# Performance work log

Measured on AMD Instinct MI355X. Metric: run time of the kernel, lower is better.

The kernel has to match this reference:

```python
import jax, jax.numpy as jnp
import numpy as np

N = 10000; E = 320000
DIM = 176; ATT = 16; SH_HEADS = 16; TH = 4; NH = SH_HEADS + TH; VD = DIM // SH_HEADS
LMAX = 3; NSPH = (LMAX + 1) ** 2; ZDIM = 16; RDIM = 16
RSTART = 0.8; CUT = 5.0; NLAYERS = 2


def _ln(x):
    mu = jnp.mean(x, axis=-1, keepdims=True)
    dx = x - mu
    var = jnp.mean(dx ** 2, axis=-1, keepdims=True)
    return dx * (1e-6 + var) ** (-0.5)


def _sph(v):
    # real spherical harmonics up to l=3, unnormalized overall scale, [E,16]
    x, y, z = v[..., 0], v[..., 1], v[..., 2]
    s3 = np.float32(np.sqrt(3.0)); s15 = np.float32(np.sqrt(15.0))
    c1 = np.float32(np.sqrt(5.0 / 8.0)); c2 = np.float32(np.sqrt(3.0 / 8.0))
    x2, y2, z2 = x * x, y * y, z * z
    return jnp.stack([
        jnp.ones_like(x),
        x, y, z,
        s3 * x * y, s3 * y * z, 0.5 * (3.0 * z2 - 1.0), s3 * x * z, 0.5 * s3 * (x2 - y2),
        c1 * y * (3.0 * x2 - y2), s15 * x * y * z, c2 * y * (5.0 * z2 - 1.0),
        0.5 * z * (5.0 * z2 - 3.0), c2 * x * (5.0 * z2 - 1.0),
        0.5 * s15 * z * (x2 - y2), c1 * x * (x2 - 3.0 * y2),
    ], axis=-1)


def setup_inputs() -> dict:
    key = jax.random.key(0)
    ks = jax.random.split(key, 32)

    def rn(k, shape):
        fan_in = shape[0] if len(shape) > 1 else shape[0]
        return jax.random.normal(k, shape, dtype=jnp.float32) / np.float32(np.sqrt(shape[0]))

    species = jax.random.randint(ks[0], (N,), 0, 64)
    edge_src = jax.random.randint(ks[1], (E,), 0, N)
    edge_dst = jax.random.randint(ks[2], (E,), 0, N)
    distances = RSTART + (CUT - RSTART) * jax.random.uniform(ks[3], (E,), dtype=jnp.float32)
    raw = jax.random.normal(ks[4], (E, 3), dtype=jnp.float32)
    dirn = raw / jnp.linalg.norm(raw, axis=-1, keepdims=True)
    vec = dirn * distances[:, None]
    switch = 0.5 * (jnp.cos(jnp.pi * distances / CUT) + 1.0)

    inp = {
        'species': species, 'distances': distances, 'switch': switch,
        'edge_src': edge_src, 'edge_dst': edge_dst, 'vec': vec,
        'z_table': jax.random.normal(ks[5], (64, ZDIM), dtype=jnp.float32),
        'w_species': rn(ks[6], (ZDIM, DIM)),
        'pos_w1_0': rn(ks[7], (RDIM, 2 * ATT)), 'pos_b1_0': jnp.zeros((2 * ATT,), jnp.float32),
        'pos_w2_0': rn(ks[8], (2 * ATT, ATT)), 'pos_b2_0': jnp.zeros((ATT,), jnp.float32),
        'wq_0': rn(ks[9], (DIM, NH * ATT)), 'wk_0': rn(ks[10], (DIM, NH * ATT)),
        'wv_0': rn(ks[11], (DIM, SH_HEADS * VD)),
        'upd_w_0': rn(ks[12], (2 * DIM, DIM)), 'upd_b_0': jnp.zeros((DIM,), jnp.float32),
        'pos_w1_1': rn(ks[13], (RDIM + TH * (LMAX + 1), 2 * ATT)), 'pos_b1_1': jnp.zeros((2 * ATT,), jnp.float32),
        'pos_w2_1': rn(ks[14], (2 * ATT, ATT)), 'pos_b2_1': jnp.zeros((ATT,), jnp.float32),
        'wq_1': rn(ks[15], (DIM, NH * ATT)), 'wk_1': rn(ks[16], (DIM, NH * ATT)),
        'wv_1': rn(ks[17], (DIM, SH_HEADS * VD)),
        'upd_w_1': rn(ks[18], (2 * DIM, DIM)), 'upd_b_1': jnp.zeros((DIM,), jnp.float32),
    }
    return inp


def reference(species, distances, switch, edge_src, edge_dst, vec,
              z_table, w_species,
              pos_w1_0, pos_b1_0, pos_w2_0, pos_b2_0, wq_0, wk_0, wv_0, upd_w_0, upd_b_0,
              pos_w1_1, pos_b1_1, pos_w2_1, pos_b2_1, wq_1, wk_1, wv_1, upd_w_1, upd_b_1):
    Nn = species.shape[0]
    Zi = z_table[species]                      # [N, ZDIM] species encoding
    xi = _ln(Zi @ w_species)                   # [N, DIM]

    vhat = vec / distances[:, None]
    Yij = _sph(vhat)                           # [E, NSPH]
    ls = np.repeat(np.arange(LMAX + 1), 2 * np.arange(LMAX + 1) + 1)
    parity = jnp.asarray(((-1.0) ** ls).astype(np.float32))  # [NSPH]

    centers = jnp.linspace(RSTART, CUT, RDIM, dtype=jnp.float32)
    sigma = np.float32((CUT - RSTART) / (RDIM - 1))
    radial = jnp.exp(-(((distances[:, None] - centers) / sigma) ** 2))  # [E, RDIM]

    Vi = jnp.zeros((Nn, TH, NSPH), jnp.float32)
    pos = [(pos_w1_0, pos_b1_0, pos_w2_0, pos_b2_0), (pos_w1_1, pos_b1_1, pos_w2_1, pos_b2_1)]
    att = [(wq_0, wk_0, wv_0, upd_w_0, upd_b_0), (wq_1, wk_1, wv_1, upd_w_1, upd_b_1)]
    inv_sqrt_d = np.float32(1.0 / np.sqrt(ATT))

    for layer in range(NLAYERS):
        pw1, pb1, pw2, pb2 = pos[layer]
        wq, wk, wv, uw, ub = att[layer]
        if layer == 0:
            ur = radial
        else:
            # tensor relative positional features: [E, TH, NSPH]
            xij2 = (Vi[edge_dst] + (parity * Vi)[edge_src]) * Yij[:, None, :]
            us = [xij2[:, :, l * l:(l + 1) * (l + 1)].sum(axis=-1) for l in range(LMAX + 1)]
            ur = jnp.concatenate([radial] + us, axis=-1)
        w = jax.nn.swish(ur @ pw1 + pb1) @ pw2 + pb2     # [E, ATT] positional encoding
        q = (xi @ wq).reshape(Nn, NH, ATT)
        k = (xi @ wk).reshape(Nn, NH, ATT)
        # multiplicative relative positional attention coefficients [E, NH]
        aij = jnp.einsum('ehd,ed->eh', q[edge_dst] * k[edge_src], w) * (switch[:, None] * inv_sqrt_d)
        a_s, a_t = aij[:, :SH_HEADS], aij[:, SH_HEADS:]
        v = (xi @ wv).reshape(Nn, SH_HEADS, VD)
        mi = jax.ops.segment_sum(a_s[:, :, None] * v[edge_src], edge_dst, num_segments=Nn)  # [N,SH,VD]
        Vi = Vi + jax.ops.segment_sum(
            a_t[:, :, None] * (Yij[:, None, :] + parity * Vi[edge_src]), edge_dst, num_segments=Nn)
        ui = jnp.concatenate([xi, mi.reshape(Nn, -1)], axis=-1)
        xi = _ln(xi + ui @ uw + ub)
    return xi
```

## Files before the change

kernel.cpp:

```cpp
#include <hip/hip_runtime.h>
#include <hip/hip_bf16.h>
#include <math.h>

#define N_NODES 10000
#define N_PAD   10048
#define N_EDGES 320000
#define DIM     176
#define ATT     16
#define SH_HEADS 16
#define THH     4
#define NH      20
#define VD      11
#define ZDIM    16
#define RDIM    16
#define QK_W    (NH*ATT)
#define QKV_W   816
#define UI_W    (2*DIM)
#define KQ      192
#define SIGINV  3.5714285714285716f
#define RSTEP   0.28f

typedef unsigned short ushort_t;
typedef __attribute__((ext_vector_type(8))) short bf16x8;
typedef __attribute__((ext_vector_type(4))) float f32x4;


__device__ __forceinline__ ushort_t f2bf(float f) {
    __hip_bfloat16 b = __float2bfloat16(f);
    return *(ushort_t*)&b;
}

__device__ __forceinline__ float bf2f(ushort_t u) {
    return __uint_as_float(((unsigned)u) << 16);
}

__device__ __forceinline__ void sph16(float x, float y, float z, float* Y) {
    const float s3  = 1.7320508075688772f;
    const float s15 = 3.872983346207417f;
    const float c1  = 0.7905694150420949f;
    const float c2  = 0.6123724356957945f;
    float x2 = x*x, y2 = y*y, z2 = z*z;
    Y[0]  = 1.0f;
    Y[1]  = x;
    Y[2]  = y;
    Y[3]  = z;
    Y[4]  = s3 * x * y;
    Y[5]  = s3 * y * z;
    Y[6]  = 0.5f * (3.0f * z2 - 1.0f);
    Y[7]  = s3 * x * z;
    Y[8]  = 0.5f * s3 * (x2 - y2);
    Y[9]  = c1 * y * (3.0f * x2 - y2);
    Y[10] = s15 * x * y * z;
    Y[11] = c2 * y * (5.0f * z2 - 1.0f);
    Y[12] = 0.5f * z * (5.0f * z2 - 3.0f);
    Y[13] = c2 * x * (5.0f * z2 - 1.0f);
    Y[14] = 0.5f * s15 * z * (x2 - y2);
    Y[15] = c1 * x * (x2 - 3.0f * y2);
}

__device__ __forceinline__ void unpack8(const uint4 u, float* f) {
    f[0] = __uint_as_float(u.x << 16);
    f[1] = __uint_as_float(u.x & 0xffff0000u);
    f[2] = __uint_as_float(u.y << 16);
    f[3] = __uint_as_float(u.y & 0xffff0000u);
    f[4] = __uint_as_float(u.z << 16);
    f[5] = __uint_as_float(u.z & 0xffff0000u);
    f[6] = __uint_as_float(u.w << 16);
    f[7] = __uint_as_float(u.w & 0xffff0000u);
}


__global__ __launch_bounds__(256) void k_deg(const int* edst, int* deg) {
    int e = blockIdx.x * 256 + threadIdx.x;
    if (e < N_EDGES) atomicAdd(&deg[edst[e]], 1);
}

__global__ __launch_bounds__(1024) void k_scan1(const int* deg, int* incl, int* bsum) {
    __shared__ int sd[1024];
    int b = blockIdx.x, tid = threadIdx.x;
    int gi = b * 1024 + tid;
    int v = (gi < N_NODES) ? deg[gi] : 0;
    sd[tid] = v;
    __syncthreads();
    for (int s = 1; s < 1024; s <<= 1) {
        int add = (tid >= s) ? sd[tid - s] : 0;
        __syncthreads();
        sd[tid] += add;
        __syncthreads();
    }
    if (gi < N_NODES) incl[gi] = sd[tid];
    if (tid == 1023) bsum[b] = sd[1023];
}

__global__ __launch_bounds__(1024) void k_scan3(const int* deg, const int* incl, const int* bsum,
                                                int* off, int* cursor) {
    __shared__ int bpre_s;
    int b = blockIdx.x, tid = threadIdx.x;
    if (tid == 0) {
        int acc = 0;
        for (int k = 0; k < b; k++) acc += bsum[k];
        bpre_s = acc;
    }
    __syncthreads();
    int gi = b * 1024 + tid;
    if (gi < N_NODES) {
        int e = bpre_s + incl[gi];
        off[gi + 1] = e;
        cursor[gi]  = e - deg[gi];
    }
    if (gi == 0) off[0] = 0;
}

__global__ __launch_bounds__(256) void k_scatter_reorder(const int* esrc, const int* edst,
        const float* dist, const float* swit, const float* vec, int* cursor,
        int* src_c, int* dst_c, float* dist_c, float* sc_c, float* Yf) {
    int e = blockIdx.x * 256 + threadIdx.x;
    if (e >= N_EDGES) return;
    int t_ = edst[e];
    int p = atomicAdd(&cursor[t_], 1);
    float d = dist[e];
    float inv = 1.0f / d;
    float vx = vec[(size_t)e*3 + 0] * inv;
    float vy = vec[(size_t)e*3 + 1] * inv;
    float vz = vec[(size_t)e*3 + 2] * inv;
    src_c[p]  = esrc[e];
    dst_c[p]  = t_;
    dist_c[p] = d;
    sc_c[p]   = swit[e] * 0.25f;
    float Y[16];
    sph16(vx, vy, vz, Y);
    #pragma unroll
    for (int m = 0; m < 16; m += 4)
        *(float4*)&Yf[(size_t)p * 16 + m] = make_float4(Y[m], Y[m+1], Y[m+2], Y[m+3]);
}


__device__ __forceinline__ void prep_qkv_body(int bid, int tid, const float* wq,
        const float* wk, const float* wv, ushort_t* Wtq) {
    int id = bid * 256 + tid;
    if (id >= 192 * 832) return;
    int k = id / 832, n = id - (id / 832) * 832;
    float v = 0.0f;
    if (k < DIM && n < QKV_W)
        v = (n < 320) ? wq[k * 320 + n] : (n < 640) ? wk[k * 320 + (n - 320)]
                                                    : wv[k * DIM + (n - 640)];
    Wtq[(size_t)n * KQ + k] = f2bf(v);
}

__device__ __forceinline__ void prep_upd_body(int bid, int tid, const float* uw, ushort_t* Wtu) {
    int id = bid * 256 + tid;
    if (id >= 352 * 192) return;
    int k = id / 192, n = id - (id / 192) * 192;
    float v = (n < DIM) ? uw[k * DIM + n] : 0.0f;
    Wtu[(size_t)n * UI_W + k] = f2bf(v);
}

__device__ __forceinline__ void prep_mlp_body(int bid, int tid, const float* pw1,
        const float* pw2, ushort_t* w1T, ushort_t* w2T, int K1) {
    int id = bid * 256 + tid;
    if (id < 1024) {
        int n = id >> 5, k = id & 31;
        w1T[n * 32 + k] = (k < K1) ? f2bf(pw1[k * 32 + n]) : 0;
    } else if (id < 1536) {
        int id2 = id - 1024;
        int n = id2 >> 5, k = id2 & 31;
        w2T[n * 32 + k] = f2bf(pw2[k * 16 + n]);
    }
}

__global__ __launch_bounds__(256) void k_prep_all(
        const float* wq0, const float* wk0, const float* wv0, ushort_t* Wtq0,
        const float* wq1, const float* wk1, const float* wv1, ushort_t* Wtq1,
        const float* uw0, ushort_t* Wtu0, const float* uw1, ushort_t* Wtu1,
        const float* pw1_0, const float* pw2_0, ushort_t* w1T0, ushort_t* w2T0,
        const float* pw1_1, const float* pw2_1, ushort_t* w1T1, ushort_t* w2T1) {
    int bid = blockIdx.x, tid = threadIdx.x;
    if (bid < 624)        prep_qkv_body(bid,        tid, wq0, wk0, wv0, Wtq0);
    else if (bid < 1248)  prep_qkv_body(bid - 624,  tid, wq1, wk1, wv1, Wtq1);
    else if (bid < 1512)  prep_upd_body(bid - 1248, tid, uw0, Wtu0);
    else if (bid < 1776)  prep_upd_body(bid - 1512, tid, uw1, Wtu1);
    else if (bid < 1782)  prep_mlp_body(bid - 1776, tid, pw1_0, pw2_0, w1T0, w2T0, 16);
    else if (bid < 1788)  prep_mlp_body(bid - 1782, tid, pw1_1, pw2_1, w1T1, w2T1, 32);
}


template<int KCHUNKS, int OMODE>
__global__ __launch_bounds__(256) void k_gemm(const ushort_t* __restrict__ A, int sA,
                                              const ushort_t* __restrict__ Bt, int sB,
                                              void* __restrict__ Cv, int sC, int M, int N,
                                              ushort_t* __restrict__ qh,
                                              ushort_t* __restrict__ kh,
                                              ushort_t* __restrict__ vh) {
    __shared__ ushort_t As[64 * 40];
    __shared__ ushort_t Bs[64 * 40];
    int tid  = threadIdx.x;
    int m0   = blockIdx.y * 64, n0 = blockIdx.x * 64;
    int w    = tid >> 6, lane = tid & 63, quad = lane >> 4, c16 = lane & 15;
    int arow = tid >> 2, aseg = tid & 3;
    f32x4 acc[4] = {};
    for (int kc = 0; kc < KCHUNKS; kc++) {
        int k0 = kc * 32;
        *(uint4*)&As[arow * 40 + aseg * 8] =
            *(const uint4*)&A[(size_t)(m0 + arow) * sA + k0 + aseg * 8];
        *(uint4*)&Bs[arow * 40 + aseg * 8] =
            *(const uint4*)&Bt[(size_t)(n0 + arow) * sB + k0 + aseg * 8];
        __syncthreads();
        bf16x8 a = *(const bf16x8*)&As[(w * 16 + c16) * 40 + quad * 8];
        #pragma unroll
        for (int t = 0; t < 4; t++) {
            bf16x8 b = *(const bf16x8*)&Bs[(t * 16 + c16) * 40 + quad * 8];
            acc[t] = __builtin_amdgcn_mfma_f32_16x16x32_bf16(a, b, acc[t], 0, 0, 0);
        }
        __syncthreads();
    }
    #pragma unroll
    for (int t = 0; t < 4; t++) {
        #pragma unroll
        for (int r = 0; r < 4; r++) {
            int row = m0 + w * 16 + quad * 4 + r;
            int col = n0 + t * 16 + c16;
            if (row < M && col < N) {
                if (OMODE == 1) {
                    ushort_t bv = f2bf(acc[t][r]);
                    if (col < 320)      qh[(size_t)row * QK_W + col] = bv;
                    else if (col < 640) kh[(size_t)row * QK_W + (col - 320)] = bv;
                    else                vh[(size_t)row * DIM  + (col - 640)] = bv;
                } else {
                    ((float*)Cv)[(size_t)row * sC + col] = acc[t][r];
                }
            }
        }
    }
}


__global__ __launch_bounds__(256) void k_node_init(const int* species, const float* z_table,
                                                   const float* wsp, float* xi,
                                                   ushort_t* xib, ushort_t* cxm) {
    __shared__ float zs[16 * ZDIM];
    __shared__ float yt[16 * DIM];
    __shared__ float red[256];
    __shared__ float mus[16], rstds[16];
    int base = blockIdx.x * 16;
    int tid  = threadIdx.x;
    { int n = tid >> 4, kk = tid & 15;
      zs[tid] = z_table[species[base + n] * ZDIM + kk]; }
    __syncthreads();
    int c = tid;
    if (c < DIM) {
        float acc[16];
        #pragma unroll
        for (int n = 0; n < 16; n++) acc[n] = 0.0f;
        for (int kk = 0; kk < ZDIM; kk++) {
            float w = wsp[kk * DIM + c];
            #pragma unroll
            for (int n = 0; n < 16; n++) acc[n] += zs[n * ZDIM + kk] * w;
        }
        #pragma unroll
        for (int n = 0; n < 16; n++) yt[n * DIM + c] = acc[n];
    }
    __syncthreads();
    { int n2 = tid >> 4, j = tid & 15;
      float s = 0.0f;
      for (int c2 = j; c2 < DIM; c2 += 16) s += yt[n2 * DIM + c2];
      red[tid] = s; }
    __syncthreads();
    if (tid < 16) { float s = 0; for (int j = 0; j < 16; j++) s += red[tid * 16 + j]; mus[tid] = s / (float)DIM; }
    __syncthreads();
    { int n2 = tid >> 4, j = tid & 15;
      float mu = mus[n2], s = 0.0f;
      for (int c2 = j; c2 < DIM; c2 += 16) { float d = yt[n2 * DIM + c2] - mu; s += d * d; }
      red[tid] = s; }
    __syncthreads();
    if (tid < 16) { float s = 0; for (int j = 0; j < 16; j++) s += red[tid * 16 + j]; rstds[tid] = rsqrtf(s / (float)DIM + 1e-6f); }
    __syncthreads();
    if (c < DIM) {
        #pragma unroll
        for (int n = 0; n < 16; n++) {
            float val = (yt[n * DIM + c] - mus[n]) * rstds[n];
            xi[(size_t)(base + n) * DIM + c] = val;
            ushort_t bv = f2bf(val);
            xib[(size_t)(base + n) * KQ + c]   = bv;
            cxm[(size_t)(base + n) * UI_W + c] = bv;
        }
    } else if (c < KQ) {
        #pragma unroll
        for (int n = 0; n < 16; n++) xib[(size_t)(base + n) * KQ + c] = 0;
    }
}


template<bool L0>
__global__ __launch_bounds__(256) void k_edge(const float* dist_c, const float* sc_c,
        const int* src_c, const int* dst_c, const float* Yf, const ushort_t* Vih,
        const ushort_t* qh, const ushort_t* kh,
        const ushort_t* w1T, const float* pb1, const ushort_t* w2T, const float* pb2,
        ushort_t* aijh) {
    __shared__ ushort_t urS[64 * 40];
    __shared__ ushort_t Ht[4][16 * 40];
    __shared__ float    wdS[64 * 17];
    __shared__ ushort_t aS[NH][64];
    int tid  = threadIdx.x;
    int w    = tid >> 6, lane = tid & 63, quad = lane >> 4, c16 = lane & 15;
    int eb   = blockIdx.x * 64;

    if (!L0) {
        if (tid < 64) {
            int i = eb + tid;
            float d = dist_c[i];
            ushort_t u[32];
            #pragma unroll
            for (int r = 0; r < 16; r++) {
                float cc = 0.8f + (float)r * RSTEP;
                float uu = (d - cc) * SIGINV;
                u[r] = f2bf(__expf(-uu * uu));
            }
            float Y[16];
            #pragma unroll
            for (int m = 0; m < 16; m += 4) {
                float4 y = *(const float4*)&Yf[(size_t)i * 16 + m];
                Y[m] = y.x; Y[m+1] = y.y; Y[m+2] = y.z; Y[m+3] = y.w;
            }
            int s = src_c[i], t_ = dst_c[i];
            const uint4* vd4 = (const uint4*)(Vih + (size_t)t_ * 64);
            const uint4* vs4 = (const uint4*)(Vih + (size_t)s  * 64);
            #pragma unroll
            for (int th = 0; th < THH; th++) {
                float fd[16], fs[16];
                unpack8(vd4[2*th],   fd);     unpack8(vd4[2*th+1], fd+8);
                unpack8(vs4[2*th],   fs);     unpack8(vs4[2*th+1], fs+8);
                float us0 = (fd[0] + fs[0]) * Y[0];
                float us1 = 0.0f, us2 = 0.0f, us3 = 0.0f;
                #pragma unroll
                for (int m = 1; m < 4; m++)  us1 += (fd[m] - fs[m]) * Y[m];
                #pragma unroll
                for (int m = 4; m < 9; m++)  us2 += (fd[m] + fs[m]) * Y[m];
                #pragma unroll
                for (int m = 9; m < 16; m++) us3 += (fd[m] - fs[m]) * Y[m];
                u[16 + 0 * 4 + th] = f2bf(us0);
                u[16 + 1 * 4 + th] = f2bf(us1);
                u[16 + 2 * 4 + th] = f2bf(us2);
                u[16 + 3 * 4 + th] = f2bf(us3);
            }
            #pragma unroll
            for (int p = 0; p < 4; p++)
                *(uint4*)&urS[tid * 40 + p * 8] = *(uint4*)&u[p * 8];
        }
        __syncthreads();
    }

    {
        int e0 = eb + w * 16;
        bf16x8 a1;
        if (L0) {
            float d = dist_c[e0 + c16];
            #pragma unroll
            for (int j = 0; j < 8; j++) {
                int r = quad * 8 + j;
                float v = 0.0f;
                if (r < 16) { float cc = 0.8f + (float)r * RSTEP; float uu = (d - cc) * SIGINV; v = __expf(-uu * uu); }
                a1[j] = (short)f2bf(v);
            }
        } else {
            a1 = *(const bf16x8*)&urS[(w * 16 + c16) * 40 + quad * 8];
        }
        bf16x8 b0 = *(const bf16x8*)&w1T[c16 * 32 + quad * 8];
        bf16x8 b1 = *(const bf16x8*)&w1T[(16 + c16) * 32 + quad * 8];
        f32x4 acc0 = {}, acc1 = {};
        acc0 = __builtin_amdgcn_mfma_f32_16x16x32_bf16(a1, b0, acc0, 0, 0, 0);
        acc1 = __builtin_amdgcn_mfma_f32_16x16x32_bf16(a1, b1, acc1, 0, 0, 0);
        float bb0 = pb1[c16], bb1 = pb1[c16 + 16];
        #pragma unroll
        for (int r = 0; r < 4; r++) {
            int er = quad * 4 + r;
            float h0 = acc0[r] + bb0; h0 = h0 / (1.0f + __expf(-h0));
            float h1 = acc1[r] + bb1; h1 = h1 / (1.0f + __expf(-h1));
            Ht[w][er * 40 + c16]      = f2bf(h0);
            Ht[w][er * 40 + 16 + c16] = f2bf(h1);
        }
        __syncthreads();
        bf16x8 a2 = *(const bf16x8*)&Ht[w][c16 * 40 + quad * 8];
        bf16x8 b2 = *(const bf16x8*)&w2T[c16 * 32 + quad * 8];
        f32x4 acc2 = {};
        acc2 = __builtin_amdgcn_mfma_f32_16x16x32_bf16(a2, b2, acc2, 0, 0, 0);
        float bb2 = pb2[c16];
        #pragma unroll
        for (int r = 0; r < 4; r++) {
            int er = quad * 4 + r;
            wdS[(w * 16 + er) * 17 + c16] = (acc2[r] + bb2) * sc_c[e0 + er];
        }
    }
    __syncthreads();

    {
        int le = tid >> 2, part = tid & 3;
        int i  = eb + le;
        int s = src_c[i], t_ = dst_c[i];
        float wd[16];
        #pragma unroll
        for (int p = 0; p < 16; p++) wd[p] = wdS[le * 17 + p];
        const uint4* q4 = (const uint4*)(qh + (size_t)t_ * QK_W);
        const uint4* k4 = (const uint4*)(kh + (size_t)s  * QK_W);
        #pragma unroll
        for (int j = 0; j < 5; j++) {
            int h = part * 5 + j;
            float qa[8], qb[8], ka[8], kb[8];
            unpack8(q4[2*h],   qa); unpack8(q4[2*h+1], qb);
            unpack8(k4[2*h],   ka); unpack8(k4[2*h+1], kb);
            float acc = 0.0f;
            #pragma unroll
            for (int dd = 0; dd < 8; dd++) acc += qa[dd] * ka[dd] * wd[dd];
            #pragma unroll
            for (int dd = 0; dd < 8; dd++) acc += qb[dd] * kb[dd] * wd[8 + dd];
            aS[h][le] = f2bf(acc);
        }
    }
    __syncthreads();
    {
        const uint* aSw = (const uint*)aS;
        for (int idx = tid; idx < NH * 32; idx += 256) {
            int h = idx >> 5, w2 = idx & 31;
            *(uint*)(aijh + (size_t)h * N_EDGES + eb + w2 * 2) = aSw[h * 32 + w2];
        }
    }
}


__device__ __forceinline__ void mi_step(int i, int c0, bool f1, bool f2,
        const int* src_c, const ushort_t* aA, const ushort_t* aB, const ushort_t* vh,
        float& acc0, float& acc1, float& acc2, float& acc3) {
    int s0 = src_c[i];
    uint2 v0 = *(const uint2*)(vh + (size_t)s0 * DIM + c0);
    float a00 = bf2f(aA[i]), a0B = bf2f(aB[i]);
    float g01 = f1 ? a0B : a00, g02 = f2 ? a0B : a00;
    acc0 += a00 * __uint_as_float(v0.x << 16);
    acc1 += g01 * __uint_as_float(v0.x & 0xffff0000u);
    acc2 += g02 * __uint_as_float(v0.y << 16);
    acc3 += a0B * __uint_as_float(v0.y & 0xffff0000u);
}

__device__ __forceinline__ void mi_wave(int n, int lane, const int* off, const int* src_c,
        const ushort_t* aijh, const ushort_t* vh, ushort_t* cxm) {
    if (lane >= 44) return;
    int c0 = lane * 4;
    int hA = c0 / VD;
    int hB = (c0 + 3) / VD;
    bool f1 = ((c0 + 1) / VD) != hA;
    bool f2 = ((c0 + 2) / VD) != hA;
    const ushort_t* aA = aijh + (size_t)hA * N_EDGES;
    const ushort_t* aB = aijh + (size_t)hB * N_EDGES;
    int start = off[n], end = off[n + 1];
    float acc0 = 0, acc1 = 0, acc2 = 0, acc3 = 0;
    int i = start;
    for (; i + 4 <= end; i += 4) {
        int s0 = src_c[i], s1 = src_c[i+1], s2 = src_c[i+2], s3 = src_c[i+3];
        uint2 v0 = *(const uint2*)(vh + (size_t)s0 * DIM + c0);
        uint2 v1 = *(const uint2*)(vh + (size_t)s1 * DIM + c0);
        uint2 v2 = *(const uint2*)(vh + (size_t)s2 * DIM + c0);
        uint2 v3 = *(const uint2*)(vh + (size_t)s3 * DIM + c0);
        float aA0 = bf2f(aA[i]),   aB0 = bf2f(aB[i]);
        float aA1 = bf2f(aA[i+1]), aB1 = bf2f(aB[i+1]);
        float aA2 = bf2f(aA[i+2]), aB2 = bf2f(aB[i+2]);
        float aA3 = bf2f(aA[i+3]), aB3 = bf2f(aB[i+3]);
        float g01 = f1 ? aB0 : aA0, g02 = f2 ? aB0 : aA0;
        float g11 = f1 ? aB1 : aA1, g12 = f2 ? aB1 : aA1;
        float g21 = f1 ? aB2 : aA2, g22 = f2 ? aB2 : aA2;
        float g31 = f1 ? aB3 : aA3, g32 = f2 ? aB3 : aA3;
        acc0 += aA0 * __uint_as_float(v0.x << 16);
        acc1 += g01 * __uint_as_float(v0.x & 0xffff0000u);
        acc2 += g02 * __uint_as_float(v0.y << 16);
        acc3 += aB0 * __uint_as_float(v0.y & 0xffff0000u);
        acc0 += aA1 * __uint_as_float(v1.x << 16);
        acc1 += g11 * __uint_as_float(v1.x & 0xffff0000u);
        acc2 += g12 * __uint_as_float(v1.y << 16);
        acc3 += aB1 * __uint_as_float(v1.y & 0xffff0000u);
        acc0 += aA2 * __uint_as_float(v2.x << 16);
        acc1 += g21 * __uint_as_float(v2.x & 0xffff0000u);
        acc2 += g22 * __uint_as_float(v2.y << 16);
        acc3 += aB2 * __uint_as_float(v2.y & 0xffff0000u);
        acc0 += aA3 * __uint_as_float(v3.x << 16);
        acc1 += g31 * __uint_as_float(v3.x & 0xffff0000u);
        acc2 += g32 * __uint_as_float(v3.y << 16);
        acc3 += aB3 * __uint_as_float(v3.y & 0xffff0000u);
    }
    for (; i < end; i++)
        mi_step(i, c0, f1, f2, src_c, aA, aB, vh, acc0, acc1, acc2, acc3);
    ushort_t o[4] = {f2bf(acc0), f2bf(acc1), f2bf(acc2), f2bf(acc3)};
    *(uint2*)(cxm + (size_t)n * UI_W + DIM + c0) = *(uint2*)o;
}

__device__ __forceinline__ void vi_wave(int n, int lane, const int* off,
        const float* Yf, const ushort_t* aijh, ushort_t* Vih) {
    int th = lane >> 4, sm = lane & 15;
    const ushort_t* ah = aijh + (size_t)(SH_HEADS + th) * N_EDGES;
    int start = off[n], end = off[n + 1];
    float acc = 0.0f;
    int i = start;
    for (; i + 4 <= end; i += 4) {
        float a0 = bf2f(ah[i]),   y0 = Yf[(size_t)i * 16 + sm];
        float a1 = bf2f(ah[i+1]), y1 = Yf[(size_t)(i+1) * 16 + sm];
        float a2 = bf2f(ah[i+2]), y2 = Yf[(size_t)(i+2) * 16 + sm];
        float a3 = bf2f(ah[i+3]), y3 = Yf[(size_t)(i+3) * 16 + sm];
        acc += a0 * y0 + a1 * y1 + a2 * y2 + a3 * y3;
    }
    for (; i < end; i++)
        acc += bf2f(ah[i]) * Yf[(size_t)i * 16 + sm];
    Vih[(size_t)n * 64 + lane] = f2bf(acc);
}

__global__ __launch_bounds__(256) void k_agg0(const int* off, const int* src_c,
        const float* Yf, const ushort_t* aijh, const ushort_t* vh,
        ushort_t* cxm, ushort_t* Vih) {
    int wid  = blockIdx.x * 4 + (threadIdx.x >> 6);
    int lane = threadIdx.x & 63;
    if (wid < N_NODES)
        mi_wave(wid, lane, off, src_c, aijh, vh, cxm);
    else
        vi_wave(wid - N_NODES, lane, off, Yf, aijh, Vih);
}

__global__ __launch_bounds__(256) void k_agg1(const int* off, const int* src_c,
        const ushort_t* aijh, const ushort_t* vh, ushort_t* cxm) {
    int wid  = blockIdx.x * 4 + (threadIdx.x >> 6);
    int lane = threadIdx.x & 63;
    mi_wave(wid, lane, off, src_c, aijh, vh, cxm);
}


__global__ __launch_bounds__(256) void k_lnfinal(const float* yg, const float* xi,
        const float* ub, float* xo, ushort_t* xib, ushort_t* cxm) {
    __shared__ float yt[16 * DIM];
    __shared__ float red[256];
    __shared__ float mus[16], rstds[16];
    int base = blockIdx.x * 16;
    int tid  = threadIdx.x;
    for (int idx = tid; idx < 16 * DIM; idx += 256) {
        int n = idx / DIM, c = idx - n * DIM;
        yt[idx] = xi[(size_t)(base + n) * DIM + c]
                + yg[(size_t)(base + n) * DIM + c] + ub[c];
    }
    __syncthreads();
    { int n2 = tid >> 4, j = tid & 15;
      float s = 0.0f;
      for (int c2 = j; c2 < DIM; c2 += 16) s += yt[n2 * DIM + c2];
      red[tid] = s; }
    __syncthreads();
    if (tid < 16) { float s = 0; for (int j = 0; j < 16; j++) s += red[tid * 16 + j]; mus[tid] = s / (float)DIM; }
    __syncthreads();
    { int n2 = tid >> 4, j = tid & 15;
      float mu = mus[n2], s = 0.0f;
      for (int c2 = j; c2 < DIM; c2 += 16) { float d = yt[n2 * DIM + c2] - mu; s += d * d; }
      red[tid] = s; }
    __syncthreads();
    if (tid < 16) { float s = 0; for (int j = 0; j < 16; j++) s += red[tid * 16 + j]; rstds[tid] = rsqrtf(s / (float)DIM + 1e-6f); }
    __syncthreads();
    int c = tid;
    if (c < DIM) {
        #pragma unroll
        for (int n = 0; n < 16; n++) {
            float val = (yt[n * DIM + c] - mus[n]) * rstds[n];
            xo[(size_t)(base + n) * DIM + c] = val;
            ushort_t bv = f2bf(val);
            xib[(size_t)(base + n) * KQ + c]   = bv;
            cxm[(size_t)(base + n) * UI_W + c] = bv;
        }
    } else if (c < KQ) {
        #pragma unroll
        for (int n = 0; n < 16; n++) xib[(size_t)(base + n) * KQ + c] = 0;
    }
}


extern "C" void kernel_launch(void* const* d_in, const int* in_sizes, int n_in,
                              void* d_out, int out_size, void* d_ws, size_t ws_size,
                              hipStream_t stream) {
    const int*   species = (const int*)  d_in[0];
    const float* dist    = (const float*)d_in[1];
    const float* swit    = (const float*)d_in[2];
    const int*   esrc    = (const int*)  d_in[3];
    const int*   edst    = (const int*)  d_in[4];
    const float* vec     = (const float*)d_in[5];
    const float* z_table = (const float*)d_in[6];
    const float* wsp     = (const float*)d_in[7];
    const float* pw1_0 = (const float*)d_in[8],  *pb1_0 = (const float*)d_in[9];
    const float* pw2_0 = (const float*)d_in[10], *pb2_0 = (const float*)d_in[11];
    const float* wq0 = (const float*)d_in[12], *wk0 = (const float*)d_in[13];
    const float* wv0 = (const float*)d_in[14], *uw0 = (const float*)d_in[15];
    const float* ub0 = (const float*)d_in[16];
    const float* pw1_1 = (const float*)d_in[17], *pb1_1 = (const float*)d_in[18];
    const float* pw2_1 = (const float*)d_in[19], *pb2_1 = (const float*)d_in[20];
    const float* wq1 = (const float*)d_in[21], *wk1 = (const float*)d_in[22];
    const float* wv1 = (const float*)d_in[23], *uw1 = (const float*)d_in[24];
    const float* ub1 = (const float*)d_in[25];
    float* out = (float*)d_out;

    char* p = (char*)d_ws;
    auto alloc = [&](size_t bytes) -> char* {
        char* r = p;
        p += (bytes + 255) & ~(size_t)255;
        return r;
    };
    int* deg    = (int*)alloc((size_t)N_NODES * 4);
    int* incl   = (int*)alloc((size_t)N_NODES * 4);
    int* bsum   = (int*)alloc(64);
    int* off    = (int*)alloc((size_t)(N_NODES + 1) * 4);
    int* cursor = (int*)alloc((size_t)N_NODES * 4);
    int*   src_c  = (int*)  alloc((size_t)N_EDGES * 4);
    int*   dst_c  = (int*)  alloc((size_t)N_EDGES * 4);
    float* dist_c = (float*)alloc((size_t)N_EDGES * 4);
    float* sc_c   = (float*)alloc((size_t)N_EDGES * 4);
    float* Yf     = (float*)alloc((size_t)N_EDGES * 16 * 4);
    float* xiA  = (float*)alloc((size_t)N_NODES * DIM * 4);
    float* xiB  = (float*)alloc((size_t)N_NODES * DIM * 4);
    ushort_t* xib  = (ushort_t*)alloc((size_t)N_PAD * KQ * 2);
    ushort_t* cxm  = (ushort_t*)alloc((size_t)N_PAD * UI_W * 2);
    ushort_t* qh   = (ushort_t*)alloc((size_t)N_NODES * QK_W * 2);
    ushort_t* kh   = (ushort_t*)alloc((size_t)N_NODES * QK_W * 2);
    ushort_t* vh   = (ushort_t*)alloc((size_t)N_NODES * DIM * 2);
    float* ybuf    = (float*)alloc((size_t)N_NODES * DIM * 4);
    ushort_t* Wtq0 = (ushort_t*)alloc((size_t)832 * KQ * 2);
    ushort_t* Wtq1 = (ushort_t*)alloc((size_t)832 * KQ * 2);
    ushort_t* Wtu0 = (ushort_t*)alloc((size_t)192 * UI_W * 2);
    ushort_t* Wtu1 = (ushort_t*)alloc((size_t)192 * UI_W * 2);
    ushort_t* w1T0 = (ushort_t*)alloc((size_t)32 * 32 * 2);
    ushort_t* w2T0 = (ushort_t*)alloc((size_t)16 * 32 * 2);
    ushort_t* w1T1 = (ushort_t*)alloc((size_t)32 * 32 * 2);
    ushort_t* w2T1 = (ushort_t*)alloc((size_t)16 * 32 * 2);
    ushort_t* Vih  = (ushort_t*)alloc((size_t)N_NODES * 64 * 2);
    ushort_t* aijh = (ushort_t*)alloc((size_t)N_EDGES * NH * 2);

    const int NB_E  = (N_EDGES + 255) / 256;
    const int NB_F  = N_EDGES / 64;
    const int NB_T  = N_NODES / 16;
    const dim3 GRID_QKV(13, 157);
    const dim3 GRID_UPD(3, 157);

    hipMemsetAsync(deg, 0, (size_t)N_NODES * 4, stream);
    k_deg<<<NB_E, 256, 0, stream>>>(edst, deg);
    k_scan1<<<10, 1024, 0, stream>>>(deg, incl, bsum);
    k_scan3<<<10, 1024, 0, stream>>>(deg, incl, bsum, off, cursor);
    k_scatter_reorder<<<NB_E, 256, 0, stream>>>(esrc, edst, dist, swit, vec, cursor,
                                                src_c, dst_c, dist_c, sc_c, Yf);

    k_prep_all<<<1788, 256, 0, stream>>>(wq0, wk0, wv0, Wtq0, wq1, wk1, wv1, Wtq1,
                                         uw0, Wtu0, uw1, Wtu1,
                                         pw1_0, pw2_0, w1T0, w2T0,
                                         pw1_1, pw2_1, w1T1, w2T1);

    k_node_init<<<NB_T, 256, 0, stream>>>(species, z_table, wsp, xiA, xib, cxm);

    k_gemm<6, 1><<<GRID_QKV, 256, 0, stream>>>(xib, KQ, Wtq0, KQ, nullptr, 0,
                                               N_NODES, QKV_W, qh, kh, vh);
    k_edge<true><<<NB_F, 256, 0, stream>>>(dist_c, sc_c, src_c, dst_c, Yf, Vih,
                                           qh, kh, w1T0, pb1_0, w2T0, pb2_0, aijh);
    k_agg0<<<5000, 256, 0, stream>>>(off, src_c, Yf, aijh, vh, cxm, Vih);
    k_gemm<11, 0><<<GRID_UPD, 256, 0, stream>>>(cxm, UI_W, Wtu0, UI_W, ybuf, DIM,
                                                N_NODES, DIM, nullptr, nullptr, nullptr);
    k_lnfinal<<<NB_T, 256, 0, stream>>>(ybuf, xiA, ub0, xiB, xib, cxm);

    k_gemm<6, 1><<<GRID_QKV, 256, 0, stream>>>(xib, KQ, Wtq1, KQ, nullptr, 0,
                                               N_NODES, QKV_W, qh, kh, vh);
    k_edge<false><<<NB_F, 256, 0, stream>>>(dist_c, sc_c, src_c, dst_c, Yf, Vih,
                                            qh, kh, w1T1, pb1_1, w2T1, pb2_1, aijh);
    k_agg1<<<2500, 256, 0, stream>>>(off, src_c, aijh, vh, cxm);
    k_gemm<11, 0><<<GRID_UPD, 256, 0, stream>>>(cxm, UI_W, Wtu1, UI_W, ybuf, DIM,
                                                N_NODES, DIM, nullptr, nullptr, nullptr);
    k_lnfinal<<<NB_T, 256, 0, stream>>>(ybuf, xiB, ub1, out, xib, cxm);
}
```

Baseline: 408.5 us.

## Store q/k head-major and spread edge prologue and attention across all threads

The QKV GEMM epilogue now writes q and k in a head-major layout ([head][node][16]) in place of node-major rows. The edge kernel's attention step assigns one head plane per wave and prefetches the next head's q/k vectors into registers. The layer-1 prologue that computed radial and tensor features on only 64 threads now splits the work across all 256 threads, one tensor head per wave. The goal is better lane utilisation and overlap of gather latency, at the cost of scattered stores in the GEMM epilogue and gathers spread over separate head planes.

```diff
diff --git a/kernel.cpp b/kernel.cpp
--- a/kernel.cpp
+++ b/kernel.cpp
@@ -222,9 +222,16 @@
             if (row < M && col < N) {
                 if (OMODE == 1) {
                     ushort_t bv = f2bf(acc[t][r]);
-                    if (col < 320)      qh[(size_t)row * QK_W + col] = bv;
-                    else if (col < 640) kh[(size_t)row * QK_W + (col - 320)] = bv;
-                    else                vh[(size_t)row * DIM  + (col - 640)] = bv;
+                    if (col < 320) {
+                        int h = col >> 4, d = col & 15;
+                        qh[((size_t)h * N_NODES + row) * 16 + d] = bv;
+                    } else if (col < 640) {
+                        int c = col - 320;
+                        int h = c >> 4, d = c & 15;
+                        kh[((size_t)h * N_NODES + row) * 16 + d] = bv;
+                    } else {
+                        vh[(size_t)row * DIM + (col - 640)] = bv;
+                    }
                 } else {
                     ((float*)Cv)[(size_t)row * sC + col] = acc[t][r];
                 }
@@ -305,47 +312,43 @@
     int eb   = blockIdx.x * 64;
 
     if (!L0) {
-        if (tid < 64) {
-            int i = eb + tid;
-            float d = dist_c[i];
-            ushort_t u[32];
-            #pragma unroll
-            for (int r = 0; r < 16; r++) {
-                float cc = 0.8f + (float)r * RSTEP;
-                float uu = (d - cc) * SIGINV;
-                u[r] = f2bf(__expf(-uu * uu));
-            }
-            float Y[16];
-            #pragma unroll
-            for (int m = 0; m < 16; m += 4) {
-                float4 y = *(const float4*)&Yf[(size_t)i * 16 + m];
-                Y[m] = y.x; Y[m+1] = y.y; Y[m+2] = y.z; Y[m+3] = y.w;
-            }
-            int s = src_c[i], t_ = dst_c[i];
-            const uint4* vd4 = (const uint4*)(Vih + (size_t)t_ * 64);
-            const uint4* vs4 = (const uint4*)(Vih + (size_t)s  * 64);
-            #pragma unroll
-            for (int th = 0; th < THH; th++) {
-                float fd[16], fs[16];
-                unpack8(vd4[2*th],   fd);     unpack8(vd4[2*th+1], fd+8);
-                unpack8(vs4[2*th],   fs);     unpack8(vs4[2*th+1], fs+8);
-                float us0 = (fd[0] + fs[0]) * Y[0];
-                float us1 = 0.0f, us2 = 0.0f, us3 = 0.0f;
-                #pragma unroll
-                for (int m = 1; m < 4; m++)  us1 += (fd[m] - fs[m]) * Y[m];
-                #pragma unroll
-                for (int m = 4; m < 9; m++)  us2 += (fd[m] + fs[m]) * Y[m];
-                #pragma unroll
-                for (int m = 9; m < 16; m++) us3 += (fd[m] - fs[m]) * Y[m];
-                u[16 + 0 * 4 + th] = f2bf(us0);
-                u[16 + 1 * 4 + th] = f2bf(us1);
-                u[16 + 2 * 4 + th] = f2bf(us2);
-                u[16 + 3 * 4 + th] = f2bf(us3);
-            }
-            #pragma unroll
-            for (int p = 0; p < 4; p++)
-                *(uint4*)&urS[tid * 40 + p * 8] = *(uint4*)&u[p * 8];
-        }
+        int e  = tid & 63, tp = tid >> 6;
+        int i  = eb + e;
+        float d = dist_c[i];
+        ushort_t ur4[4];
+        #pragma unroll
+        for (int r0 = 0; r0 < 4; r0++) {
+            int r = tp * 4 + r0;
+            float cc = 0.8f + (float)r * RSTEP;
+            float uu = (d - cc) * SIGINV;
+            ur4[r0] = f2bf(__expf(-uu * uu));
+        }
+        *(uint2*)&urS[e * 40 + tp * 4] = *(uint2*)ur4;
+        float Y[16];
+        #pragma unroll
+        for (int m = 0; m < 16; m += 4) {
+            float4 y = *(const float4*)&Yf[(size_t)i * 16 + m];
+            Y[m] = y.x; Y[m+1] = y.y; Y[m+2] = y.z; Y[m+3] = y.w;
+        }
+        int s = src_c[i], t_ = dst_c[i];
+        const uint4* vd4 = (const uint4*)(Vih + (size_t)t_ * 64);
+        const uint4* vs4 = (const uint4*)(Vih + (size_t)s  * 64);
+        int th = tp;
+        float fd[16], fs[16];
+        unpack8(vd4[2*th],   fd);     unpack8(vd4[2*th+1], fd+8);
+        unpack8(vs4[2*th],   fs);     unpack8(vs4[2*th+1], fs+8);
+        float us0 = (fd[0] + fs[0]) * Y[0];
+        float us1 = 0.0f, us2 = 0.0f, us3 = 0.0f;
+        #pragma unroll
+        for (int m = 1; m < 4; m++)  us1 += (fd[m] - fs[m]) * Y[m];
+        #pragma unroll
+        for (int m = 4; m < 9; m++)  us2 += (fd[m] + fs[m]) * Y[m];
+        #pragma unroll
+        for (int m = 9; m < 16; m++) us3 += (fd[m] - fs[m]) * Y[m];
+        urS[e * 40 + 16 + 0 * 4 + th] = f2bf(us0);
+        urS[e * 40 + 16 + 1 * 4 + th] = f2bf(us1);
+        urS[e * 40 + 16 + 2 * 4 + th] = f2bf(us2);
+        urS[e * 40 + 16 + 3 * 4 + th] = f2bf(us3);
         __syncthreads();
     }
 
@@ -393,26 +396,41 @@
     __syncthreads();
 
     {
-        int le = tid >> 2, part = tid & 3;
+        int le = tid & 63, w4 = tid >> 6;
         int i  = eb + le;
         int s = src_c[i], t_ = dst_c[i];
         float wd[16];
         #pragma unroll
         for (int p = 0; p < 16; p++) wd[p] = wdS[le * 17 + p];
-        const uint4* q4 = (const uint4*)(qh + (size_t)t_ * QK_W);
-        const uint4* k4 = (const uint4*)(kh + (size_t)s  * QK_W);
-        #pragma unroll
-        for (int j = 0; j < 5; j++) {
-            int h = part * 5 + j;
-            float qa[8], qb[8], ka[8], kb[8];
-            unpack8(q4[2*h],   qa); unpack8(q4[2*h+1], qb);
-            unpack8(k4[2*h],   ka); unpack8(k4[2*h+1], kb);
+        const ushort_t* qrow = qh + (size_t)t_ * 16;
+        const ushort_t* krow = kh + (size_t)s  * 16;
+        const size_t PL = (size_t)N_NODES * 16;
+        size_t o0 = (size_t)w4 * PL;
+        uint4 qa = *(const uint4*)(qrow + o0);
+        uint4 qb = *(const uint4*)(qrow + o0 + 8);
+        uint4 ka = *(const uint4*)(krow + o0);
+        uint4 kb = *(const uint4*)(krow + o0 + 8);
+        #pragma unroll
+        for (int it = 0; it < 5; it++) {
+            int h = it * 4 + w4;
+            uint4 nqa, nqb, nka, nkb;
+            if (it < 4) {
+                size_t o = (size_t)(h + 4) * PL;
+                nqa = *(const uint4*)(qrow + o);
+                nqb = *(const uint4*)(qrow + o + 8);
+                nka = *(const uint4*)(krow + o);
+                nkb = *(const uint4*)(krow + o + 8);
+            }
+            float qaf[8], qbf[8], kaf[8], kbf[8];
+            unpack8(qa, qaf); unpack8(qb, qbf);
+            unpack8(ka, kaf); unpack8(kb, kbf);
             float acc = 0.0f;
             #pragma unroll
-            for (int dd = 0; dd < 8; dd++) acc += qa[dd] * ka[dd] * wd[dd];
+            for (int dd = 0; dd < 8; dd++) acc += qaf[dd] * kaf[dd] * wd[dd];
             #pragma unroll
-            for (int dd = 0; dd < 8; dd++) acc += qb[dd] * kb[dd] * wd[8 + dd];
+            for (int dd = 0; dd < 8; dd++) acc += qbf[dd] * kbf[dd] * wd[8 + dd];
             aS[h][le] = f2bf(acc);
+            if (it < 4) { qa = nqa; qb = nqb; ka = nka; kb = nkb; }
         }
     }
     __syncthreads();
```

New measurement: 451.9 us. 1.11x slower.
